# Kernel tuning notes

Measured on AMD Instinct MI355X. Metric: run time of the kernel, lower is better.

Reference implementation:

```python
import jax, jax.numpy as jnp
import numpy as np

TOP_K = 2
SCALING = 32.0 / 64.0  # lora_alpha / reservoir_size


def setup_inputs() -> dict:
    key = jax.random.key(0)
    ks = jax.random.split(key, 6)
    Bsz, S, Din, Dout, R, E = 4, 2048, 4096, 4096, 64, 16
    x = jax.random.normal(ks[0], (Bsz, S, Din), dtype=jnp.float32)
    base_w = jax.random.normal(ks[1], (Dout, Din), dtype=jnp.float32) * 0.02
    base_b = jax.random.normal(ks[2], (Dout,), dtype=jnp.float32) * 0.02
    A = jax.random.normal(ks[3], (R, Din), dtype=jnp.float32) * (1.0 / np.sqrt(Din))
    B = jax.random.normal(ks[4], (E, Dout, R), dtype=jnp.float32) * 0.02
    router_w = jax.random.normal(ks[5], (E, Din), dtype=jnp.float32) * 0.02
    return {"x": x, "base_w": base_w, "base_b": base_b, "A": A, "B": B, "router_w": router_w}


def reference(x, base_w, base_b, A, B, router_w):
    # base linear: [b,s,din] @ [dout,din]^T + bias
    base_out = jnp.einsum('bsi,oi->bso', x, base_w) + base_b
    # low-rank projection through fixed reservoir A (activation=identity, dropout off)
    res_hidden = jnp.einsum('bsi,ri->bsr', x, A)          # [b,s,r]
    # routing
    logits = jnp.einsum('bsi,ei->bse', x, router_w)       # [b,s,E]
    probs = jax.nn.softmax(logits, axis=-1)
    topw, topi = jax.lax.top_k(probs, TOP_K)              # [b,s,k]
    topw = topw / (jnp.sum(topw, axis=-1, keepdims=True) + 1e-6)
    num_experts = B.shape[0]
    # combine weights per expert: sum_k w_k * onehot(idx_k)  -> [b,s,E]
    combine = jnp.sum(jax.nn.one_hot(topi, num_experts, dtype=x.dtype) * topw[..., None], axis=-2)
    # weighted per-expert lowrank B matmul and combine
    delta = jnp.einsum('bse,bsr,eor->bso', combine, res_hidden, B)
    return base_out + delta * SCALING
```

## Files before the change

kernel.cpp:

```cpp
#include <hip/hip_runtime.h>
#include <cstdint>
#include <cstddef>

typedef short short8 __attribute__((ext_vector_type(8)));
typedef float f32x4 __attribute__((ext_vector_type(4)));
typedef float f32x16 __attribute__((ext_vector_type(16)));

#define DIN  4096
#define DOUT 4096
#define RANK 64
#define NEXP 16
#define NTOK 8192
#define KCAT 5120

__device__ __forceinline__ unsigned short f2bf(float f) {
    unsigned int u = __builtin_bit_cast(unsigned int, f);
    u = (u + 0x7FFFu + ((u >> 16) & 1u)) >> 16;
    return (unsigned short)u;
}
__device__ __forceinline__ void async_cp16(const void* g, void* lds) {
    __builtin_amdgcn_global_load_lds(
        (const __attribute__((address_space(1))) void*)g,
        (__attribute__((address_space(3))) void*)lds, 16, 0, 0);
}

__global__ void __launch_bounds__(256) prep_all_kernel(
        const float* __restrict__ x, const float* __restrict__ rw,
        const float* __restrict__ bw, const float* __restrict__ Bm,
        const float* __restrict__ Am,
        unsigned short* __restrict__ Xcat, unsigned short* __restrict__ Wcat,
        unsigned short* __restrict__ W1A, float* __restrict__ Lg) {
    __shared__ __align__(16) float xsl[8][532];
    __shared__ __align__(16) float red[8][16][16];
    const int tid = threadIdx.x;

    if (blockIdx.x < 1024) {
        const int t0 = blockIdx.x * 8;
        const int tt = tid >> 5, l32 = tid & 31;
        const int eg = tid >> 6, ts = (tid >> 4) & 3, cc = tid & 15;
        float part[2][4] = {};

        for (int w = 0; w < 8; ++w) {
            #pragma unroll
            for (int sub = 0; sub < 4; ++sub) {
                const int col = w * 512 + sub * 128 + l32 * 4;
                const float4 xv = *(const float4*)&x[(size_t)(t0 + tt) * DIN + col];
                unsigned short b0 = f2bf(xv.x), b1 = f2bf(xv.y),
                               b2 = f2bf(xv.z), b3 = f2bf(xv.w);
                uint2 pk = { (unsigned)b0 | ((unsigned)b1 << 16),
                             (unsigned)b2 | ((unsigned)b3 << 16) };
                *(uint2*)&Xcat[(size_t)(t0 + tt) * KCAT + col] = pk;
                *(float4*)&xsl[tt][sub * 128 + l32 * 4] = xv;
            }
            __syncthreads();
            #pragma unroll
            for (int j = 0; j < 8; ++j) {
                const int colb = w * 512 + (j * 16 + cc) * 4;
                const float4 r0 = *(const float4*)&rw[(size_t)(eg * 4 + 0) * DIN + colb];
                const float4 r1 = *(const float4*)&rw[(size_t)(eg * 4 + 1) * DIN + colb];
                const float4 r2 = *(const float4*)&rw[(size_t)(eg * 4 + 2) * DIN + colb];
                const float4 r3 = *(const float4*)&rw[(size_t)(eg * 4 + 3) * DIN + colb];
                #pragma unroll
                for (int t2 = 0; t2 < 2; ++t2) {
                    const int t = ts * 2 + t2;
                    const float4 xv = *(const float4*)&xsl[t][(j * 16 + cc) * 4];
                    part[t2][0] += xv.x * r0.x + xv.y * r0.y + xv.z * r0.z + xv.w * r0.w;
                    part[t2][1] += xv.x * r1.x + xv.y * r1.y + xv.z * r1.z + xv.w * r1.w;
                    part[t2][2] += xv.x * r2.x + xv.y * r2.y + xv.z * r2.z + xv.w * r2.w;
                    part[t2][3] += xv.x * r3.x + xv.y * r3.y + xv.z * r3.z + xv.w * r3.w;
                }
            }
            __syncthreads();
        }
        #pragma unroll
        for (int t2 = 0; t2 < 2; ++t2)
            #pragma unroll
            for (int e = 0; e < 4; ++e)
                red[ts * 2 + t2][eg * 4 + e][cc] = part[t2][e];
        __syncthreads();
        if (tid < 128) {
            const int t = tid >> 4, e = tid & 15;
            float s = 0.f;
            #pragma unroll
            for (int c = 0; c < 16; ++c) s += red[t][e][c];
            Lg[(size_t)(t0 + t) * NEXP + e] = s;
        }
    } else {
        const unsigned NG1 = (unsigned)DOUT * KCAT / 8u;
        const unsigned NGT = NG1 + 64u * DIN / 8u;
        for (unsigned g = (blockIdx.x - 1024) * 256u + tid; g < NGT;
             g += 2048u * 256u) {
            const float* src;
            unsigned short* dst;
            if (g < NG1) {
                unsigned o  = g / 640u;
                unsigned c8 = (g - o * 640u) * 8u;
                dst = Wcat + (size_t)o * KCAT + c8;
                if (c8 < DIN) {
                    src = bw + (size_t)o * DIN + c8;
                } else {
                    unsigned cc2 = c8 - DIN;
                    unsigned e = cc2 >> 6, r = cc2 & 63u;
                    src = Bm + ((size_t)e * DOUT + o) * RANK + r;
                }
            } else {
                unsigned g2 = g - NG1;
                unsigned row = g2 >> 9;
                unsigned c8  = (g2 & 511u) * 8u;
                dst = W1A + (size_t)row * DIN + c8;
                src = Am + (size_t)row * DIN + c8;
            }
            float4 v0 = *(const float4*)(src);
            float4 v1 = *(const float4*)(src + 4);
            uint4 pk;
            pk.x = (unsigned)f2bf(v0.x) | ((unsigned)f2bf(v0.y) << 16);
            pk.y = (unsigned)f2bf(v0.z) | ((unsigned)f2bf(v0.w) << 16);
            pk.z = (unsigned)f2bf(v1.x) | ((unsigned)f2bf(v1.y) << 16);
            pk.w = (unsigned)f2bf(v1.z) | ((unsigned)f2bf(v1.w) << 16);
            *(uint4*)dst = pk;
        }
    }
}

__global__ void __launch_bounds__(256) proj_moe_kernel(
        const unsigned short* __restrict__ Xcat,
        const unsigned short* __restrict__ W1A,
        const float* __restrict__ Lg, unsigned short* __restrict__ XcatW) {
    __shared__ __align__(16) unsigned short Xs[16 * 128];
    __shared__ __align__(16) unsigned short Ws[64 * 128];
    __shared__ __align__(16) float cw[16][16];
    __shared__ __align__(16) float hbuf[16][68];
    const int tid = threadIdx.x;
    const int wave = tid >> 6, lane = tid & 63;
    const int quad = lane >> 4, l16 = lane & 15;
    const int t0 = blockIdx.x * 16;

    const int rX = tid >> 4, cXs = tid & 15;
    const int cX = (cXs & 8) | ((cXs ^ rX) & 7);

    if (tid < 16) {
        float l[16];
        #pragma unroll
        for (int e = 0; e < 16; ++e) l[e] = Lg[(size_t)(t0 + tid) * NEXP + e];
        int i1 = 0; float b1v = l[0];
        #pragma unroll
        for (int e = 1; e < 16; ++e) if (l[e] > b1v) { b1v = l[e]; i1 = e; }
        int i2 = -1; float b2v = -1e30f;
        #pragma unroll
        for (int e = 0; e < 16; ++e) if (e != i1 && l[e] > b2v) { b2v = l[e]; i2 = e; }
        float S = 0.f;
        #pragma unroll
        for (int e = 0; e < 16; ++e) S += expf(l[e] - b1v);
        const float p1 = 1.0f / S;
        const float p2 = expf(b2v - b1v) / S;
        const float d = p1 + p2 + 1e-6f;
        const float c1 = 0.5f * p1 / d;
        const float c2 = 0.5f * p2 / d;
        #pragma unroll
        for (int e = 0; e < 16; ++e)
            cw[tid][e] = (e == i1) ? c1 : (e == i2) ? c2 : 0.0f;
    }

    f32x4 acc = {};
    for (int kt = 0; kt < DIN / 128; ++kt) {
        const int k0 = kt * 128;
        async_cp16(Xcat + (size_t)(t0 + rX) * KCAT + k0 + cX * 8,
                   (char*)Xs + wave * 1024);
        #pragma unroll
        for (int i = 0; i < 4; ++i) {
            const int s = i * 256 + tid;
            const int rW = s >> 4, cWs = s & 15;
            const int cWc = (cWs & 8) | ((cWs ^ rW) & 7);
            async_cp16(W1A + (size_t)rW * DIN + k0 + cWc * 8,
                       (char*)Ws + i * 4096 + wave * 1024);
        }
        __syncthreads();
        #pragma unroll
        for (int kk = 0; kk < 4; ++kk) {
            const int c = kk * 4 + quad;
            const int sa = ((c & 8) | ((c ^ l16) & 7)) << 3;
            const int rb = wave * 16 + l16;
            const int sb = ((c & 8) | ((c ^ rb) & 7)) << 3;
            short8 am = *(const short8*)&Xs[l16 * 128 + sa];
            short8 bn = *(const short8*)&Ws[rb * 128 + sb];
            acc = __builtin_amdgcn_mfma_f32_16x16x32_bf16(am, bn, acc, 0, 0, 0);
        }
        __syncthreads();
    }
    #pragma unroll
    for (int r = 0; r < 4; ++r)
        hbuf[quad * 4 + r][wave * 16 + l16] = acc[r];
    __syncthreads();
    const int t = tid >> 4, e = tid & 15;
    const float c = cw[t][e];
    unsigned short* dst = XcatW + (size_t)(t0 + t) * KCAT + DIN + e * 64;
    #pragma unroll
    for (int r8 = 0; r8 < 8; ++r8) {
        unsigned short o16[8];
        #pragma unroll
        for (int k = 0; k < 8; ++k)
            o16[k] = f2bf(c * hbuf[t][r8 * 8 + k]);
        uint4 pk;
        pk.x = (unsigned)o16[0] | ((unsigned)o16[1] << 16);
        pk.y = (unsigned)o16[2] | ((unsigned)o16[3] << 16);
        pk.z = (unsigned)o16[4] | ((unsigned)o16[5] << 16);
        pk.w = (unsigned)o16[6] | ((unsigned)o16[7] << 16);
        *(uint4*)(dst + r8 * 8) = pk;
    }
}

__global__ void __launch_bounds__(256) gemm_main_kernel(
        const unsigned short* __restrict__ Xcat,
        const unsigned short* __restrict__ Wcat,
        const float* __restrict__ bias, float* __restrict__ out) {
    __shared__ __align__(16) unsigned short Xs[128 * 64];
    __shared__ __align__(16) unsigned short Ws[128 * 64];
    const int tid = threadIdx.x;
    const int wave = tid >> 6, lane = tid & 63;
    const int half = lane >> 5, l32 = lane & 31;
    const int bn0 = blockIdx.x * 128;
    const int bm0 = blockIdx.y * 128;
    const int srow = tid >> 3;
    const int scol = ((tid & 7) ^ (srow & 7)) * 8;
    const unsigned short* gx = Xcat + (size_t)(bm0 + srow) * KCAT + scol;
    const unsigned short* gw = Wcat + (size_t)(bn0 + srow) * KCAT + scol;
    const int wm0 = (wave & 1) * 64;
    const int wn0 = (wave >> 1) * 64;
    f32x16 acc[2][2] = {};
    for (int kt = 0; kt < KCAT / 64; ++kt) {
        const int k0 = kt * 64;
        #pragma unroll
        for (int i = 0; i < 4; ++i) {
            async_cp16(gx + (size_t)(i * 32) * KCAT + k0, (char*)Xs + i * 4096 + wave * 1024);
            async_cp16(gw + (size_t)(i * 32) * KCAT + k0, (char*)Ws + i * 4096 + wave * 1024);
        }
        __syncthreads();
        #pragma unroll
        for (int kk2 = 0; kk2 < 4; ++kk2) {
            const int c = kk2 * 2 + half;
            short8 am[2], bn[2];
            #pragma unroll
            for (int i = 0; i < 2; ++i) {
                const int r = wm0 + i * 32 + l32;
                am[i] = *(const short8*)&Xs[r * 64 + ((c ^ (r & 7)) << 3)];
            }
            #pragma unroll
            for (int j = 0; j < 2; ++j) {
                const int r = wn0 + j * 32 + l32;
                bn[j] = *(const short8*)&Ws[r * 64 + ((c ^ (r & 7)) << 3)];
            }
            #pragma unroll
            for (int i = 0; i < 2; ++i)
                #pragma unroll
                for (int j = 0; j < 2; ++j)
                    acc[i][j] = __builtin_amdgcn_mfma_f32_32x32x16_bf16(
                        am[i], bn[j], acc[i][j], 0, 0, 0);
        }
        __syncthreads();
    }
    #pragma unroll
    for (int j = 0; j < 2; ++j) {
        const int col = bn0 + wn0 + j * 32 + l32;
        const float bj = bias[col];
        #pragma unroll
        for (int i = 0; i < 2; ++i) {
            const int rb = bm0 + wm0 + i * 32 + 4 * half;
            #pragma unroll
            for (int r = 0; r < 16; ++r) {
                const int row = rb + (r & 3) + 8 * (r >> 2);
                out[(size_t)row * DOUT + col] = acc[i][j][r] + bj;
            }
        }
    }
}

extern "C" void kernel_launch(void* const* d_in, const int* in_sizes, int n_in,
                              void* d_out, int out_size, void* d_ws, size_t ws_size,
                              hipStream_t stream) {
    const float* x  = (const float*)d_in[0];
    const float* bw = (const float*)d_in[1];
    const float* bb = (const float*)d_in[2];
    const float* Am = (const float*)d_in[3];
    const float* Bm = (const float*)d_in[4];
    const float* rw = (const float*)d_in[5];
    float* out = (float*)d_out;
    char* ws = (char*)d_ws;
    unsigned short* Xcat = (unsigned short*)(ws);
    unsigned short* Wcat = (unsigned short*)(ws + 83886080);
    unsigned short* W1A  = (unsigned short*)(ws + 125829120);
    float* Lg = (float*)(ws + 126353408);

    hipLaunchKernelGGL(prep_all_kernel, dim3(3072),   dim3(256), 0, stream,
                       x, rw, bw, Bm, Am, Xcat, Wcat, W1A, Lg);
    hipLaunchKernelGGL(proj_moe_kernel, dim3(512),    dim3(256), 0, stream,
                       Xcat, W1A, Lg, Xcat);
    hipLaunchKernelGGL(gemm_main_kernel, dim3(32, 64), dim3(256), 0, stream,
                       Xcat, Wcat, bb, out);
}
```

Measured before the change: 700.8 us.

## Rewrite main GEMM with 256x256 tiles, double-buffered async loads and block swizzle

The main bf16 GEMM moves from 128x128 tiles with 4 waves and a single LDS buffer to 256x256 tiles with 8 waves, using 16x16x32 MFMA. Global-to-LDS async copies are double-buffered and interleaved with the MFMA phases, with explicit waitcnt, barriers and setprio. Blocks are remapped so neighbours share operand tiles in L2. The aim is to hide load latency and raise reuse per byte loaded, at the cost of 128KB of LDS, more register pressure and tricky manual synchronisation.

```diff
diff --git a/kernel.cpp b/kernel.cpp
--- a/kernel.cpp
+++ b/kernel.cpp
@@ -4,7 +4,6 @@
 
 typedef short short8 __attribute__((ext_vector_type(8)));
 typedef float f32x4 __attribute__((ext_vector_type(4)));
-typedef float f32x16 __attribute__((ext_vector_type(16)));
 
 #define DIN  4096
 #define DOUT 4096
@@ -12,6 +11,7 @@
 #define NEXP 16
 #define NTOK 8192
 #define KCAT 5120
+#define NKT  (KCAT / 64)
 
 __device__ __forceinline__ unsigned short f2bf(float f) {
     unsigned int u = __builtin_bit_cast(unsigned int, f);
@@ -209,68 +209,132 @@
     }
 }
 
-__global__ void __launch_bounds__(256) gemm_main_kernel(
+__global__ void __launch_bounds__(512, 2) gemm_main_kernel(
         const unsigned short* __restrict__ Xcat,
         const unsigned short* __restrict__ Wcat,
         const float* __restrict__ bias, float* __restrict__ out) {
-    __shared__ __align__(16) unsigned short Xs[128 * 64];
-    __shared__ __align__(16) unsigned short Ws[128 * 64];
-    const int tid = threadIdx.x;
+    __shared__ __align__(16) unsigned short As[2][256 * 64];
+    __shared__ __align__(16) unsigned short Bs[2][256 * 64];
+
+    const int tid  = threadIdx.x;
     const int wave = tid >> 6, lane = tid & 63;
-    const int half = lane >> 5, l32 = lane & 31;
-    const int bn0 = blockIdx.x * 128;
-    const int bm0 = blockIdx.y * 128;
-    const int srow = tid >> 3;
-    const int scol = ((tid & 7) ^ (srow & 7)) * 8;
-    const unsigned short* gx = Xcat + (size_t)(bm0 + srow) * KCAT + scol;
-    const unsigned short* gw = Wcat + (size_t)(bn0 + srow) * KCAT + scol;
-    const int wm0 = (wave & 1) * 64;
-    const int wn0 = (wave >> 1) * 64;
-    f32x16 acc[2][2] = {};
-    for (int kt = 0; kt < KCAT / 64; ++kt) {
-        const int k0 = kt * 64;
-        #pragma unroll
-        for (int i = 0; i < 4; ++i) {
-            async_cp16(gx + (size_t)(i * 32) * KCAT + k0, (char*)Xs + i * 4096 + wave * 1024);
-            async_cp16(gw + (size_t)(i * 32) * KCAT + k0, (char*)Ws + i * 4096 + wave * 1024);
-        }
-        __syncthreads();
-        #pragma unroll
-        for (int kk2 = 0; kk2 < 4; ++kk2) {
-            const int c = kk2 * 2 + half;
-            short8 am[2], bn[2];
-            #pragma unroll
-            for (int i = 0; i < 2; ++i) {
-                const int r = wm0 + i * 32 + l32;
-                am[i] = *(const short8*)&Xs[r * 64 + ((c ^ (r & 7)) << 3)];
-            }
-            #pragma unroll
-            for (int j = 0; j < 2; ++j) {
-                const int r = wn0 + j * 32 + l32;
-                bn[j] = *(const short8*)&Ws[r * 64 + ((c ^ (r & 7)) << 3)];
-            }
-            #pragma unroll
-            for (int i = 0; i < 2; ++i)
+    const int l16  = lane & 15, quad = lane >> 4;
+    const int wm   = wave >> 2, wn = wave & 3;
+
+    const int bid = blockIdx.x;
+    const int swz = (bid & 7) * 64 + (bid >> 3);
+    const int bm0 = (swz & 31) * 256;
+    const int bn0 = (swz >> 5) * 256;
+
+    const int urr = tid >> 3;
+    const int cks = (tid & 7) ^ (urr & 7);
+    const unsigned short* sA[2][2];
+    const unsigned short* sB[2][2];
+    #pragma unroll
+    for (int h = 0; h < 2; ++h) {
+        sA[h][0] = Xcat + (size_t)(bm0 +       h * 64 + urr) * KCAT + cks * 8;
+        sA[h][1] = Xcat + (size_t)(bm0 + 128 + h * 64 + urr) * KCAT + cks * 8;
+    }
+    #pragma unroll
+    for (int u = 0; u < 2; ++u) {
+        sB[u][0] = Wcat + (size_t)(bn0 + u * 128 +      urr) * KCAT + cks * 8;
+        sB[u][1] = Wcat + (size_t)(bn0 + u * 128 + 64 + urr) * KCAT + cks * 8;
+    }
+
+    auto stageA = [&](unsigned short* buf, int h, int tt) {
+        async_cp16(sA[h][0] + (size_t)tt * 64,
+                   (char*)(buf + (h * 1024 +       wave * 64) * 8));
+        async_cp16(sA[h][1] + (size_t)tt * 64,
+                   (char*)(buf + (h * 1024 + 512 + wave * 64) * 8));
+    };
+    auto stageB = [&](unsigned short* buf, int u, int tt) {
+        async_cp16(sB[u][0] + (size_t)tt * 64,
+                   (char*)(buf + (u * 1024 +       wave * 64) * 8));
+        async_cp16(sB[u][1] + (size_t)tt * 64,
+                   (char*)(buf + (u * 1024 + 512 + wave * 64) * 8));
+    };
+
+    const int cko0 = ((quad)     ^ (l16 & 7)) * 8;
+    const int cko1 = ((4 + quad) ^ (l16 & 7)) * 8;
+    int arow[8], brow[4];
+    #pragma unroll
+    for (int m = 0; m < 8; ++m)
+        arow[m] = ((m >> 2) * 128 + wm * 64 + (m & 3) * 16 + l16) * 64;
+    #pragma unroll
+    for (int n = 0; n < 4; ++n)
+        brow[n] = (wn * 64 + n * 16 + l16) * 64;
+
+    f32x4 acc[8][4] = {};
+    short8 bf[4][2];
+
+    stageB(Bs[0], 0, 0); stageB(Bs[0], 1, 0);
+    stageA(As[0], 0, 0); stageA(As[0], 1, 0);
+    stageB(Bs[1], 0, 1); stageB(Bs[1], 1, 1);
+    stageA(As[1], 0, 1);
+    asm volatile("s_waitcnt vmcnt(6)" ::: "memory");
+    __builtin_amdgcn_s_barrier();
+
+    for (int t = 0; t < NKT; ++t) {
+        const int b = t & 1;
+        const unsigned short* pA = As[b];
+        const unsigned short* pB = Bs[b];
+        unsigned short* Acur  = As[b];
+        unsigned short* Anext = As[b ^ 1];
+        unsigned short* Bcur  = Bs[b];
+        const int ts1 = (t + 1 < NKT) ? t + 1 : t;
+        const int ts2 = (t + 2 < NKT) ? t + 2 : t;
+
+        #pragma unroll
+        for (int q = 0; q < 4; ++q) {
+            short8 af[2][2];
+            if (q == 0) {
                 #pragma unroll
-                for (int j = 0; j < 2; ++j)
-                    acc[i][j] = __builtin_amdgcn_mfma_f32_32x32x16_bf16(
-                        am[i], bn[j], acc[i][j], 0, 0, 0);
-        }
-        __syncthreads();
-    }
-    #pragma unroll
-    for (int j = 0; j < 2; ++j) {
-        const int col = bn0 + wn0 + j * 32 + l32;
+                for (int n = 0; n < 4; ++n) {
+                    bf[n][0] = *(const short8*)&pB[brow[n] + cko0];
+                    bf[n][1] = *(const short8*)&pB[brow[n] + cko1];
+                }
+            }
+            #pragma unroll
+            for (int mm = 0; mm < 2; ++mm) {
+                af[mm][0] = *(const short8*)&pA[arow[2 * q + mm] + cko0];
+                af[mm][1] = *(const short8*)&pA[arow[2 * q + mm] + cko1];
+            }
+            if      (q == 0) stageA(Anext, 1, ts1);
+            else if (q == 1) stageB(Bcur, 0, ts2);
+            else if (q == 2) stageB(Bcur, 1, ts2);
+            else             stageA(Acur, 0, ts2);
+
+            asm volatile("" ::: "memory");
+            __builtin_amdgcn_s_barrier();
+            asm volatile("s_waitcnt lgkmcnt(0)" ::: "memory");
+            __builtin_amdgcn_sched_barrier(0);
+            __builtin_amdgcn_s_setprio(1);
+            #pragma unroll
+            for (int kk = 0; kk < 2; ++kk)
+                #pragma unroll
+                for (int mm = 0; mm < 2; ++mm)
+                    #pragma unroll
+                    for (int n = 0; n < 4; ++n)
+                        acc[2 * q + mm][n] = __builtin_amdgcn_mfma_f32_16x16x32_bf16(
+                            af[mm][kk], bf[n][kk], acc[2 * q + mm][n], 0, 0, 0);
+            __builtin_amdgcn_s_setprio(0);
+            __builtin_amdgcn_sched_barrier(0);
+            if (q == 3) asm volatile("s_waitcnt vmcnt(6)" ::: "memory");
+            asm volatile("" ::: "memory");
+            __builtin_amdgcn_s_barrier();
+        }
+    }
+
+    const int orow = bm0 + wm * 128 + quad * 4;
+    #pragma unroll
+    for (int n = 0; n < 4; ++n) {
+        const int col = bn0 + wn * 64 + n * 16 + l16;
         const float bj = bias[col];
         #pragma unroll
-        for (int i = 0; i < 2; ++i) {
-            const int rb = bm0 + wm0 + i * 32 + 4 * half;
-            #pragma unroll
-            for (int r = 0; r < 16; ++r) {
-                const int row = rb + (r & 3) + 8 * (r >> 2);
-                out[(size_t)row * DOUT + col] = acc[i][j][r] + bj;
-            }
-        }
+        for (int m = 0; m < 8; ++m)
+            #pragma unroll
+            for (int r = 0; r < 4; ++r)
+                out[(size_t)(orow + m * 16 + r) * DOUT + col] = acc[m][n][r] + bj;
     }
 }
 
@@ -294,6 +358,6 @@
                        x, rw, bw, Bm, Am, Xcat, Wcat, W1A, Lg);
     hipLaunchKernelGGL(proj_moe_kernel, dim3(512),    dim3(256), 0, stream,
                        Xcat, W1A, Lg, Xcat);
-    hipLaunchKernelGGL(gemm_main_kernel, dim3(32, 64), dim3(256), 0, stream,
+    hipLaunchKernelGGL(gemm_main_kernel, dim3(512),   dim3(512), 0, stream,
                        Xcat, Wcat, bb, out);
 }
```

Result: slower. 719.6 us (+2.7%).

## Rewrite main GEMM with 256x256 tiles, double-buffered async LDS pipeline

Applied to the files above, without the earlier changes.

Replaces the 128x128 single-buffered bf16 GEMM with a 256x256 tile kernel run by 512 threads (8 waves). It double-buffers LDS and interleaves async global-to-LDS staging with MFMA phases, adding register fragment prefetch, s_setprio around MFMA and a swizzled block order for L2 locality. The aim is to hide global load latency, raise arithmetic intensity and cut barrier stalls in the dominant GEMM. It needs 128KB of LDS and large accumulator register use, and the hand-placed waitcnt and barrier ordering risks races.

```diff
diff --git a/kernel.cpp b/kernel.cpp
--- a/kernel.cpp
+++ b/kernel.cpp
@@ -12,6 +12,8 @@
 #define NEXP 16
 #define NTOK 8192
 #define KCAT 5120
+#define NKT  (KCAT / 64)
+#define ROWB (KCAT * 2)
 
 __device__ __forceinline__ unsigned short f2bf(float f) {
     unsigned int u = __builtin_bit_cast(unsigned int, f);
@@ -209,69 +211,149 @@
     }
 }
 
-__global__ void __launch_bounds__(256) gemm_main_kernel(
+__global__ void __launch_bounds__(512, 2) gemm_main_kernel(
         const unsigned short* __restrict__ Xcat,
         const unsigned short* __restrict__ Wcat,
         const float* __restrict__ bias, float* __restrict__ out) {
-    __shared__ __align__(16) unsigned short Xs[128 * 64];
-    __shared__ __align__(16) unsigned short Ws[128 * 64];
-    const int tid = threadIdx.x;
+    __shared__ __align__(16) unsigned short As[2][256 * 64];
+    __shared__ __align__(16) unsigned short Bs[2][256 * 64];
+
+    const int tid  = threadIdx.x;
     const int wave = tid >> 6, lane = tid & 63;
-    const int half = lane >> 5, l32 = lane & 31;
-    const int bn0 = blockIdx.x * 128;
-    const int bm0 = blockIdx.y * 128;
-    const int srow = tid >> 3;
-    const int scol = ((tid & 7) ^ (srow & 7)) * 8;
-    const unsigned short* gx = Xcat + (size_t)(bm0 + srow) * KCAT + scol;
-    const unsigned short* gw = Wcat + (size_t)(bn0 + srow) * KCAT + scol;
-    const int wm0 = (wave & 1) * 64;
-    const int wn0 = (wave >> 1) * 64;
-    f32x16 acc[2][2] = {};
-    for (int kt = 0; kt < KCAT / 64; ++kt) {
-        const int k0 = kt * 64;
-        #pragma unroll
-        for (int i = 0; i < 4; ++i) {
-            async_cp16(gx + (size_t)(i * 32) * KCAT + k0, (char*)Xs + i * 4096 + wave * 1024);
-            async_cp16(gw + (size_t)(i * 32) * KCAT + k0, (char*)Ws + i * 4096 + wave * 1024);
-        }
-        __syncthreads();
-        #pragma unroll
-        for (int kk2 = 0; kk2 < 4; ++kk2) {
-            const int c = kk2 * 2 + half;
-            short8 am[2], bn[2];
-            #pragma unroll
-            for (int i = 0; i < 2; ++i) {
-                const int r = wm0 + i * 32 + l32;
-                am[i] = *(const short8*)&Xs[r * 64 + ((c ^ (r & 7)) << 3)];
-            }
-            #pragma unroll
-            for (int j = 0; j < 2; ++j) {
-                const int r = wn0 + j * 32 + l32;
-                bn[j] = *(const short8*)&Ws[r * 64 + ((c ^ (r & 7)) << 3)];
-            }
-            #pragma unroll
-            for (int i = 0; i < 2; ++i)
-                #pragma unroll
-                for (int j = 0; j < 2; ++j)
-                    acc[i][j] = __builtin_amdgcn_mfma_f32_32x32x16_bf16(
-                        am[i], bn[j], acc[i][j], 0, 0, 0);
-        }
-        __syncthreads();
-    }
+    const int r5   = lane & 31, hi = lane >> 5, xb = r5 & 7;
+    const int wm   = wave >> 2, wn = wave & 3;
+
+    const int bid = blockIdx.x;
+    const int swz = (bid & 7) * 64 + (bid >> 3);
+    const int bm0 = (swz & 31) * 256;
+    const int bn0 = (swz >> 5) * 256;
+
+    const int urr = tid >> 3;
+    const int cks = (tid & 7) ^ (urr & 7);
+    const unsigned voffG = (unsigned)(urr * KCAT + cks * 8) * 2u;
+
+    const char* gA = (const char*)Xcat + (size_t)bm0 * ROWB + voffG;
+    const char* gB = (const char*)Wcat + (size_t)bn0 * ROWB + voffG;
+    char* const ldsA  = (char*)&As[0][0];
+    char* const ldsB  = (char*)&Bs[0][0];
+    char* const ldswA = ldsA + wave * 1024;
+    char* const ldswB = ldsB + wave * 1024;
+
+#define STAGE_A(H, TT, BOFF2) { \
+    async_cp16(gA + (size_t)((H) * 64) * ROWB + (size_t)(TT) * 128, \
+               ldswA + (BOFF2) + (H) * 8192); \
+    async_cp16(gA + (size_t)((H) * 64 + 128) * ROWB + (size_t)(TT) * 128, \
+               ldswA + (BOFF2) + (H) * 8192 + 16384); }
+#define STAGE_B(U, TT, BOFF2) { \
+    async_cp16(gB + (size_t)((U) * 128) * ROWB + (size_t)(TT) * 128, \
+               ldswB + (BOFF2) + (U) * 16384); \
+    async_cp16(gB + (size_t)((U) * 128 + 64) * ROWB + (size_t)(TT) * 128, \
+               ldswB + (BOFF2) + (U) * 16384 + 8192); }
+
+    int vA[4], vB[4];
     #pragma unroll
-    for (int j = 0; j < 2; ++j) {
-        const int col = bn0 + wn0 + j * 32 + l32;
-        const float bj = bias[col];
-        #pragma unroll
-        for (int i = 0; i < 2; ++i) {
-            const int rb = bm0 + wm0 + i * 32 + 4 * half;
-            #pragma unroll
-            for (int r = 0; r < 16; ++r) {
-                const int row = rb + (r & 3) + 8 * (r >> 2);
-                out[(size_t)row * DOUT + col] = acc[i][j][r] + bj;
-            }
-        }
-    }
+    for (int kk = 0; kk < 4; ++kk) {
+        const int vb = r5 * 128 + (((2 * kk + hi) ^ xb) * 16);
+        vA[kk] = vb + wm * 8192;
+        vB[kk] = vb + wn * 8192;
+    }
+
+    f32x16 acc00 = {}, acc01 = {}, acc10 = {}, acc11 = {};
+    f32x16 acc20 = {}, acc21 = {}, acc30 = {}, acc31 = {};
+    short8 bf0[4], bf1[4], fE[4], fO[4];
+
+#define PREF_AF(DST, Q, BOFF2) { \
+    _Pragma("unroll") \
+    for (int kk = 0; kk < 4; ++kk) \
+        DST[kk] = *(const short8*)(ldsA + (BOFF2) + vA[kk] + \
+                                   ((Q) >> 1) * 16384 + ((Q) & 1) * 4096); }
+#define MFMA8(AF, A0, A1) { \
+    __builtin_amdgcn_s_setprio(1); \
+    _Pragma("unroll") \
+    for (int kk = 0; kk < 4; ++kk) { \
+        A0 = __builtin_amdgcn_mfma_f32_32x32x16_bf16(AF[kk], bf0[kk], A0, 0, 0, 0); \
+        A1 = __builtin_amdgcn_mfma_f32_32x32x16_bf16(AF[kk], bf1[kk], A1, 0, 0, 0); \
+    } \
+    __builtin_amdgcn_s_setprio(0); }
+#define CLOB asm volatile("" ::: "memory")
+#define BAR  __builtin_amdgcn_s_barrier()
+#define LGKM0 { asm volatile("s_waitcnt lgkmcnt(0)" ::: "memory"); \
+                __builtin_amdgcn_sched_barrier(0); }
+#define SBAR __builtin_amdgcn_sched_barrier(0)
+
+    STAGE_B(0, 0, 0);     STAGE_B(1, 0, 0);
+    STAGE_A(0, 0, 0);     STAGE_A(1, 0, 0);
+    STAGE_B(0, 1, 32768); STAGE_B(1, 1, 32768);
+    STAGE_A(0, 1, 32768);
+    asm volatile("s_waitcnt vmcnt(6)" ::: "memory");
+    CLOB; BAR; CLOB;
+
+    #pragma unroll 2
+    for (int t = 0; t < NKT; ++t) {
+        const int boff = (t & 1) * 32768;
+        const int ob   = boff ^ 32768;
+        const int ts1  = (t + 1 < NKT) ? t + 1 : t;
+        const int ts2  = (t + 2 < NKT) ? t + 2 : t;
+
+        #pragma unroll
+        for (int kk = 0; kk < 4; ++kk) {
+            bf0[kk] = *(const short8*)(ldsB + boff + vB[kk]);
+            bf1[kk] = *(const short8*)(ldsB + boff + vB[kk] + 4096);
+            fE[kk]  = *(const short8*)(ldsA + boff + vA[kk]);
+        }
+        STAGE_A(1, ts1, ob);
+        CLOB; BAR;
+        LGKM0;
+        PREF_AF(fO, 1, boff); SBAR;
+        MFMA8(fE, acc00, acc01);
+        SBAR; CLOB; BAR;
+
+        STAGE_B(0, ts2, boff);
+        CLOB; BAR;
+        LGKM0;
+        PREF_AF(fE, 2, boff); SBAR;
+        MFMA8(fO, acc10, acc11);
+        SBAR; CLOB; BAR;
+
+        STAGE_B(1, ts2, boff);
+        CLOB; BAR;
+        LGKM0;
+        PREF_AF(fO, 3, boff); SBAR;
+        MFMA8(fE, acc20, acc21);
+        SBAR; CLOB; BAR;
+
+        STAGE_A(0, ts2, boff);
+        CLOB; BAR;
+        LGKM0;
+        MFMA8(fO, acc30, acc31);
+        SBAR;
+        asm volatile("s_waitcnt vmcnt(6)" ::: "memory");
+        CLOB; BAR;
+    }
+
+#define EPI(Q, A0, A1) { \
+    const int rb = bm0 + ((Q) >> 1) * 128 + wm * 64 + ((Q) & 1) * 32 + 4 * hi; \
+    { const int col = bn0 + wn * 64 + r5; const float bj = bias[col]; \
+      _Pragma("unroll") for (int r = 0; r < 16; ++r) { \
+        const int row = rb + (r & 3) + 8 * (r >> 2); \
+        out[(size_t)row * DOUT + col] = A0[r] + bj; } } \
+    { const int col = bn0 + wn * 64 + 32 + r5; const float bj = bias[col]; \
+      _Pragma("unroll") for (int r = 0; r < 16; ++r) { \
+        const int row = rb + (r & 3) + 8 * (r >> 2); \
+        out[(size_t)row * DOUT + col] = A1[r] + bj; } } }
+    EPI(0, acc00, acc01)
+    EPI(1, acc10, acc11)
+    EPI(2, acc20, acc21)
+    EPI(3, acc30, acc31)
+#undef STAGE_A
+#undef STAGE_B
+#undef PREF_AF
+#undef MFMA8
+#undef CLOB
+#undef BAR
+#undef LGKM0
+#undef SBAR
+#undef EPI
 }
 
 extern "C" void kernel_launch(void* const* d_in, const int* in_sizes, int n_in,
@@ -294,6 +376,6 @@
                        x, rw, bw, Bm, Am, Xcat, Wcat, W1A, Lg);
     hipLaunchKernelGGL(proj_moe_kernel, dim3(512),    dim3(256), 0, stream,
                        Xcat, W1A, Lg, Xcat);
-    hipLaunchKernelGGL(gemm_main_kernel, dim3(32, 64), dim3(256), 0, stream,
+    hipLaunchKernelGGL(gemm_main_kernel, dim3(512),   dim3(512), 0, stream,
                        Xcat, Wcat, bb, out);
 }
```

After: 660.6 us. -5.7%, faster.
